# Kernel optimization log

Measured on AMD Instinct MI355X. Metric: run time of the kernel, lower is better.

Reference implementation:

```python
import jax, jax.numpy as jnp
import numpy as np

KERNEL_SIZE = 3   # init kwarg kernel_size
BATCHSIZE = 4     # init kwarg batchsize (true output batch; bs = num * BATCHSIZE)


def setup_inputs() -> dict:
    key = jax.random.key(0)
    k1, k2, k3 = jax.random.split(key, 3)
    num = 4                      # candidate flows per image
    bs = num * BATCHSIZE         # 16
    ds, hs, ws = 256, 64, 64
    hf, wf = 64, 64
    source = jax.random.normal(k1, (bs, ds, hs, ws), dtype=jnp.float32)
    # flows with realistic magnitude (a few pixels of displacement)
    flow_field = jax.random.normal(k2, (bs, 2, hf, wf), dtype=jnp.float32) * 8.0
    masks = jax.random.uniform(k3, (bs, 1, hf, wf), dtype=jnp.float32)
    return {"source": source, "flow_field": flow_field, "masks": masks}


def _bilinear_sample_zero(img, y, x):
    """img: (C,H,W); y,x: (Ho,Wo) continuous coords. Zero outside bounds."""
    C, H, W = img.shape
    y0 = jnp.floor(y).astype(jnp.int32)
    x0 = jnp.floor(x).astype(jnp.int32)
    out = jnp.zeros((C,) + y.shape, img.dtype)
    for dy in (0, 1):
        for dx in (0, 1):
            yi = y0 + dy
            xi = x0 + dx
            w = (1.0 - jnp.abs(y - yi)) * (1.0 - jnp.abs(x - xi))
            valid = (yi >= 0) & (yi < H) & (xi >= 0) & (xi < W)
            v = img[:, jnp.clip(yi, 0, H - 1), jnp.clip(xi, 0, W - 1)]  # (C,Ho,Wo)
            out = out + jnp.where(valid, w, 0.0)[None] * v
    return out


def reference(source, flow_field, masks):
    k, B = KERNEL_SIZE, BATCHSIZE
    bs, ds, hs, ws = source.shape
    hf, wf = flow_field.shape[2], flow_field.shape[3]
    num = bs // B
    Ho, Wo = k * hf, k * wf

    ys = jnp.arange(Ho)
    xs = jnp.arange(Wo)
    ysrc = ys // k              # which flow cell each output row belongs to
    xsrc = xs // k
    yoff = (ys % k) - (k // 2)  # centered in-block offset
    xoff = (xs % k) - (k // 2)

    # expand per-cell flow to per-output-pixel: (bs, Ho, Wo)
    fy = flow_field[:, 0][:, ysrc][:, :, xsrc]
    fx = flow_field[:, 1][:, ysrc][:, :, xsrc]
    py = ysrc.astype(fy.dtype)[:, None] + yoff.astype(fy.dtype)[:, None] + fy
    px = xsrc.astype(fx.dtype)[None, :] + xoff.astype(fx.dtype)[None, :] + fx

    sampled = jax.vmap(_bilinear_sample_zero)(source, py, px)  # (bs, ds, Ho, Wo)

    # per-cell mask broadcast over the kxk block and channels
    m = masks[:, :, ysrc][:, :, :, xsrc]  # (bs, 1, Ho, Wo)
    weighted = sampled * m

    # accumulate the num candidate flows into the true batch
    out = weighted.reshape(num, B, ds, Ho, Wo).sum(axis=0)
    return out
```

## Files before the change

kernel.cpp:

```cpp
#include <hip/hip_runtime.h>

#define DS 256
#define HS 64
#define WS 64
#define BOUT 4
#define NUM 4
#define HO 192
#define WO 192

__global__ __launch_bounds__(256, 2)
void mbe_kernel(const float* __restrict__ src,
                const float* __restrict__ flow,
                const float* __restrict__ masks,
                float* __restrict__ out)
{
    const int d  = blockIdx.x;
    const int bo = blockIdx.y;
    const int tid = threadIdx.x;

    __shared__ float img[NUM][HS * WS];

    #pragma unroll
    for (int n = 0; n < NUM; ++n) {
        const float4* g = (const float4*)(src + (((size_t)(n * BOUT + bo) * DS + d) * (size_t)(HS * WS)));
        float4* s = (float4*)img[n];
        #pragma unroll
        for (int it = 0; it < 4; ++it)
            s[it * 256 + tid] = g[it * 256 + tid];
    }
    __syncthreads();

    const size_t obase = ((size_t)bo * DS + d) * (size_t)(HO * WO);

    for (int it = 0; it < 16; ++it) {
        const int g  = it * 256 + tid;
        const int ys = g >> 6;
        const int xs = g & 63;
        const int fidx = (ys << 6) + xs;

        float acc[3][3];
        #pragma unroll
        for (int j = 0; j < 3; ++j)
            #pragma unroll
            for (int i = 0; i < 3; ++i)
                acc[j][i] = 0.0f;

        #pragma unroll
        for (int n = 0; n < NUM; ++n) {
            const int b = n * BOUT + bo;
            const float fy = flow[((size_t)(b * 2 + 0) << 12) + fidx];
            const float fx = flow[((size_t)(b * 2 + 1) << 12) + fidx];
            const float m  = masks[((size_t)b << 12) + fidx];

            const float gy = (float)ys + fy;
            const float gx = (float)xs + fx;
            const float fiy = floorf(gy);
            const float fix = floorf(gx);
            const int iy = (int)fiy;
            const int ix = (int)fix;
            const float ty = gy - fiy;
            const float tx = gx - fix;

            float hx[4][3];
            #pragma unroll
            for (int r = 0; r < 4; ++r) {
                const int yy = iy - 1 + r;
                const bool yv = (yy >= 0) & (yy < HS);
                const int yyc = min(max(yy, 0), HS - 1);
                float v[4];
                #pragma unroll
                for (int c = 0; c < 4; ++c) {
                    const int xx = ix - 1 + c;
                    const bool ok = yv & (xx >= 0) & (xx < WS);
                    const int xxc = min(max(xx, 0), WS - 1);
                    const float lv = img[n][yyc * WS + xxc];
                    v[c] = ok ? lv : 0.0f;
                }
                #pragma unroll
                for (int i = 0; i < 3; ++i)
                    hx[r][i] = v[i] + tx * (v[i + 1] - v[i]);
            }

            const float wy1 = m * ty;
            const float wy0 = m - wy1;
            #pragma unroll
            for (int j = 0; j < 3; ++j)
                #pragma unroll
                for (int i = 0; i < 3; ++i)
                    acc[j][i] += wy0 * hx[j][i] + wy1 * hx[j + 1][i];
        }

        #pragma unroll
        for (int j = 0; j < 3; ++j) {
            const int yo = 3 * ys + j;
            #pragma unroll
            for (int i = 0; i < 3; ++i) {
                const int xo = 3 * xs + i;
                out[obase + (size_t)yo * WO + xo] = acc[j][i];
            }
        }
    }
}

extern "C" void kernel_launch(void* const* d_in, const int* in_sizes, int n_in,
                              void* d_out, int out_size, void* d_ws, size_t ws_size,
                              hipStream_t stream) {
    const float* src   = (const float*)d_in[0];
    const float* flow  = (const float*)d_in[1];
    const float* masks = (const float*)d_in[2];
    float* out = (float*)d_out;

    dim3 grid(DS, BOUT);
    mbe_kernel<<<grid, 256, 0, stream>>>(src, flow, masks, out);
}
```

Before: 279.6 us.

## Use 512-thread blocks with dynamic LDS, hoisted flow loads and padded x addressing

Doubles the block size to 512 threads with a launch bound of 4 blocks, and moves the 64KB image tile into dynamic shared memory with a 4-float guard pad. The pad lets each row read contiguous x offsets without per-element clamping. Flow and mask loads for all candidates are hoisted ahead of the compute loop, and bounds checks use unsigned compares. This aims to cut address arithmetic and expose more memory-level parallelism. It may raise register pressure and reduce the number of resident blocks.

```diff
diff --git a/kernel.cpp b/kernel.cpp
--- a/kernel.cpp
+++ b/kernel.cpp
@@ -7,36 +7,48 @@
 #define NUM 4
 #define HO 192
 #define WO 192
+#define NTHREADS 512
+#define IMG_FLOATS (NUM * HS * WS)
+#define LDS_FLOATS (IMG_FLOATS + 8)
 
-__global__ __launch_bounds__(256, 2)
+__global__ __launch_bounds__(NTHREADS, 4)
 void mbe_kernel(const float* __restrict__ src,
                 const float* __restrict__ flow,
                 const float* __restrict__ masks,
                 float* __restrict__ out)
 {
+    extern __shared__ float lds[];
+    float* img = lds + 4;
+
     const int d  = blockIdx.x;
     const int bo = blockIdx.y;
     const int tid = threadIdx.x;
 
-    __shared__ float img[NUM][HS * WS];
-
     #pragma unroll
     for (int n = 0; n < NUM; ++n) {
         const float4* g = (const float4*)(src + (((size_t)(n * BOUT + bo) * DS + d) * (size_t)(HS * WS)));
-        float4* s = (float4*)img[n];
+        float4* s = (float4*)(img + n * (HS * WS));
         #pragma unroll
-        for (int it = 0; it < 4; ++it)
-            s[it * 256 + tid] = g[it * 256 + tid];
+        for (int it = 0; it < 2; ++it)
+            s[it * NTHREADS + tid] = g[it * NTHREADS + tid];
     }
     __syncthreads();
 
     const size_t obase = ((size_t)bo * DS + d) * (size_t)(HO * WO);
 
-    for (int it = 0; it < 16; ++it) {
-        const int g  = it * 256 + tid;
+    for (int it = 0; it < 8; ++it) {
+        const int g  = it * NTHREADS + tid;
         const int ys = g >> 6;
         const int xs = g & 63;
-        const int fidx = (ys << 6) + xs;
+
+        float fy[NUM], fx[NUM], mm[NUM];
+        #pragma unroll
+        for (int n = 0; n < NUM; ++n) {
+            const int b = n * BOUT + bo;
+            fy[n] = flow[((size_t)(b * 2 + 0) << 12) + g];
+            fx[n] = flow[((size_t)(b * 2 + 1) << 12) + g];
+            mm[n] = masks[((size_t)b << 12) + g];
+        }
 
         float acc[3][3];
         #pragma unroll
@@ -47,13 +59,8 @@
 
         #pragma unroll
         for (int n = 0; n < NUM; ++n) {
-            const int b = n * BOUT + bo;
-            const float fy = flow[((size_t)(b * 2 + 0) << 12) + fidx];
-            const float fx = flow[((size_t)(b * 2 + 1) << 12) + fidx];
-            const float m  = masks[((size_t)b << 12) + fidx];
-
-            const float gy = (float)ys + fy;
-            const float gx = (float)xs + fx;
+            const float gy = (float)ys + fy[n];
+            const float gx = (float)xs + fx[n];
             const float fiy = floorf(gy);
             const float fix = floorf(gx);
             const int iy = (int)fiy;
@@ -61,28 +68,35 @@
             const float ty = gy - fiy;
             const float tx = gx - fix;
 
+            const int ixm1 = ix - 1;
+            const int ixc  = min(max(ixm1, -3), 63);
+            bool xv[4];
+            #pragma unroll
+            for (int c = 0; c < 4; ++c)
+                xv[c] = ((unsigned)(ixm1 + c) < (unsigned)WS);
+
+            const float* imgn = img + n * (HS * WS);
+
             float hx[4][3];
             #pragma unroll
             for (int r = 0; r < 4; ++r) {
                 const int yy = iy - 1 + r;
-                const bool yv = (yy >= 0) & (yy < HS);
+                const bool yv = ((unsigned)yy < (unsigned)HS);
                 const int yyc = min(max(yy, 0), HS - 1);
+                const float* p = imgn + yyc * WS + ixc;
                 float v[4];
                 #pragma unroll
                 for (int c = 0; c < 4; ++c) {
-                    const int xx = ix - 1 + c;
-                    const bool ok = yv & (xx >= 0) & (xx < WS);
-                    const int xxc = min(max(xx, 0), WS - 1);
-                    const float lv = img[n][yyc * WS + xxc];
-                    v[c] = ok ? lv : 0.0f;
+                    const float lv = p[c];
+                    v[c] = (yv & xv[c]) ? lv : 0.0f;
                 }
                 #pragma unroll
                 for (int i = 0; i < 3; ++i)
                     hx[r][i] = v[i] + tx * (v[i + 1] - v[i]);
             }
 
-            const float wy1 = m * ty;
-            const float wy0 = m - wy1;
+            const float wy1 = mm[n] * ty;
+            const float wy0 = mm[n] - wy1;
             #pragma unroll
             for (int j = 0; j < 3; ++j)
                 #pragma unroll
@@ -110,6 +124,14 @@
     const float* masks = (const float*)d_in[2];
     float* out = (float*)d_out;
 
+    const size_t shmem = LDS_FLOATS * sizeof(float);
+    static bool attr_set = false;
+    if (!attr_set) {
+        hipFuncSetAttribute((const void*)mbe_kernel,
+                            hipFuncAttributeMaxDynamicSharedMemorySize, (int)shmem);
+        attr_set = true;
+    }
+
     dim3 grid(DS, BOUT);
-    mbe_kernel<<<grid, 256, 0, stream>>>(src, flow, masks, out);
+    mbe_kernel<<<grid, NTHREADS, shmem, stream>>>(src, flow, masks, out);
 }
```

Measured after the change: 237.0 us. 1.18x faster.
